# Kernel tuning notes

Hardware: AMD Instinct MI355X
Metric: run time of the kernel (lower is better)

Reference implementation:

```python
import jax, jax.numpy as jnp
import numpy as np

Q_MAX = 127.0  # int8 symmetric quantization range

def _ste_round(v):
    # straight-through round (matches quantize-forward semantics)
    return v + jax.lax.stop_gradient(jnp.round(v) - v)

def setup_inputs() -> dict:
    key = jax.random.key(0)
    k1, k2, k3, k4 = jax.random.split(key, 4)
    B, S, D_IN, D_OUT = 32, 577, 1024, 2560
    x = jax.random.normal(k1, (B, S, D_IN), dtype=jnp.float32)
    # pre-quantized int8 weight stored as int32 for jax friendliness
    w_int = jax.random.randint(k2, (D_OUT, D_IN), -127, 128, dtype=jnp.int32)
    # per-output-row dequant scales (absmax/127 style, small positive)
    scale_w = jax.random.uniform(k3, (D_OUT,), dtype=jnp.float32, minval=0.005, maxval=0.02)
    bias = jax.random.normal(k4, (D_OUT,), dtype=jnp.float32)
    return {"x": x, "w_int": w_int, "scale_w": scale_w, "bias": bias}

def reference(x, w_int, scale_w, bias):
    # bnb Int8Linear: dynamic per-row int8 quantization of activations,
    # per-column (output-feature) weight scales, then bias add.
    # x: [B, S, D_in], w_int: [D_out, D_in] in [-127,127], scale_w: [D_out]
    absmax_x = jnp.max(jnp.abs(x), axis=-1, keepdims=True)  # [B, S, 1]
    scale_x = jnp.maximum(absmax_x, 1e-8) / Q_MAX
    x_q = _ste_round(x / scale_x)  # quantized activations in [-127, 127]
    # integer-valued GEMM carried in fp32 accumulation
    acc = jnp.einsum("bsd,od->bso", x_q, w_int.astype(jnp.float32))
    y = acc * scale_x * scale_w[None, None, :] + bias[None, None, :]
    return y
```

## Files before the change

### kernel.cpp

```cpp
#include <hip/hip_runtime.h>
#include <stdint.h>

typedef int v4i  __attribute__((ext_vector_type(4)));
typedef int v16i __attribute__((ext_vector_type(16)));

__device__ __forceinline__ void gll16(const void* g, void* l) {
    __builtin_amdgcn_global_load_lds(
        (const __attribute__((address_space(1))) void*)(uintptr_t)g,
        (__attribute__((address_space(3))) void*)(uint32_t)(uintptr_t)l,
        16, 0, 0);
}

__global__ __launch_bounds__(256) void quant_x(const float* __restrict__ x,
                                               signed char* __restrict__ xq,
                                               float* __restrict__ sx, int M) {
    const int row = blockIdx.x;
    const int tid = threadIdx.x;
    signed char* qrow = xq + (size_t)row * 1024;
    if (row >= M) {
        ((char4*)qrow)[tid] = make_char4(0, 0, 0, 0);
        if (tid == 0) sx[row] = 0.0f;
        return;
    }
    const float4 v = ((const float4*)(x + (size_t)row * 1024))[tid];
    float a = fmaxf(fmaxf(fabsf(v.x), fabsf(v.y)), fmaxf(fabsf(v.z), fabsf(v.w)));
#pragma unroll
    for (int off = 32; off > 0; off >>= 1)
        a = fmaxf(a, __shfl_xor(a, off));
    __shared__ float red[4];
    if ((tid & 63) == 0) red[tid >> 6] = a;
    __syncthreads();
    const float am = fmaxf(fmaxf(red[0], red[1]), fmaxf(red[2], red[3]));
    const float amc = fmaxf(am, 1e-8f);
    const float scale = amc * (1.0f / 127.0f);
    const float inv = 127.0f / amc;
    char4 q;
    q.x = (signed char)(int)rintf(v.x * inv);
    q.y = (signed char)(int)rintf(v.y * inv);
    q.z = (signed char)(int)rintf(v.z * inv);
    q.w = (signed char)(int)rintf(v.w * inv);
    ((char4*)qrow)[tid] = q;
    if (tid == 0) sx[row] = scale;
}

__global__ __launch_bounds__(256) void conv_w(const int* __restrict__ w,
                                              signed char* __restrict__ w8, int n4) {
    const int i = blockIdx.x * 256 + threadIdx.x;
    if (i < n4) {
        const int4 v = ((const int4*)w)[i];
        char4 c;
        c.x = (signed char)v.x; c.y = (signed char)v.y;
        c.z = (signed char)v.z; c.w = (signed char)v.w;
        ((char4*)w8)[i] = c;
    }
}

__global__ __launch_bounds__(256, 3) void gemm_i8(const signed char* __restrict__ xq,
                                                  const signed char* __restrict__ w8,
                                                  const float* __restrict__ sx,
                                                  const float* __restrict__ sw,
                                                  const float* __restrict__ bias,
                                                  float* __restrict__ out,
                                                  int M, int N, int K) {
    __shared__ signed char As[2][8192];
    __shared__ signed char Bs[2][8192];

    const int tid  = threadIdx.x;
    const int lane = tid & 63;
    const int wave = tid >> 6;
    const int m_off = (wave >> 1) * 64;
    const int n_off = (wave & 1) * 64;
    const int m_block = blockIdx.y * 128;
    const int n_block = blockIdx.x * 128;
    const int NT = K >> 6;

    v16i acc[2][2];
#pragma unroll
    for (int mi = 0; mi < 2; ++mi)
#pragma unroll
        for (int ni = 0; ni < 2; ++ni)
#pragma unroll
            for (int e = 0; e < 16; ++e) acc[mi][ni][e] = 0;

    const int sr = tid >> 2;
    const int sc = ((tid & 3) ^ ((sr >> 1) & 3)) * 16;
    const signed char* aG = xq + (size_t)(m_block + sr) * K + sc;
    const signed char* bG = w8 + (size_t)(n_block + sr) * K + sc;
    const int ldst = wave * 1024;

    auto stage = [&](int Tt, int b) {
        const size_t ko = (size_t)Tt << 6;
        gll16(aG + ko,                    &As[b][ldst]);
        gll16(aG + ko + ((size_t)K << 6), &As[b][ldst + 4096]);
        gll16(bG + ko,                    &Bs[b][ldst]);
        gll16(bG + ko + ((size_t)K << 6), &Bs[b][ldst + 4096]);
    };

    const int rl  = lane & 31;
    const int hi  = lane >> 5;
    const int key = (rl >> 1) & 3;
    const int ck0 = (hi ^ key) * 16;
    const int ck1 = ((2 + hi) ^ key) * 16;
    const int arow = (m_off + rl) * 64;
    const int brow = (n_off + rl) * 64;

    stage(0, 0);
    stage(1, 1);
    asm volatile("s_waitcnt vmcnt(4)" ::: "memory");
    __builtin_amdgcn_s_barrier();

    v4i a0, a1, b0, b1;
    v4i na0, na1, nb0, nb1;
    a0 = *(const v4i*)(As[0] + arow + ck0);
    a1 = *(const v4i*)(As[0] + arow + 2048 + ck0);
    b0 = *(const v4i*)(Bs[0] + brow + ck0);
    b1 = *(const v4i*)(Bs[0] + brow + 2048 + ck0);

    for (int T = 0; T < NT; ++T) {
        const int cur = T & 1;
        const signed char* Ac = As[cur];
        const signed char* Bc = Bs[cur];
        na0 = *(const v4i*)(Ac + arow + ck1);
        na1 = *(const v4i*)(Ac + arow + 2048 + ck1);
        nb0 = *(const v4i*)(Bc + brow + ck1);
        nb1 = *(const v4i*)(Bc + brow + 2048 + ck1);

        acc[0][0] = __builtin_amdgcn_mfma_i32_32x32x32_i8(a0, b0, acc[0][0], 0, 0, 0);
        acc[0][1] = __builtin_amdgcn_mfma_i32_32x32x32_i8(a0, b1, acc[0][1], 0, 0, 0);
        acc[1][0] = __builtin_amdgcn_mfma_i32_32x32x32_i8(a1, b0, acc[1][0], 0, 0, 0);
        acc[1][1] = __builtin_amdgcn_mfma_i32_32x32x32_i8(a1, b1, acc[1][1], 0, 0, 0);

        asm volatile("s_waitcnt lgkmcnt(0)" ::: "memory");
        __builtin_amdgcn_s_barrier();

        if (T + 2 < NT) stage(T + 2, cur);

        if (T + 1 < NT) {
            if (T + 2 < NT)
                asm volatile("s_waitcnt vmcnt(4)" ::: "memory");
            else
                asm volatile("s_waitcnt vmcnt(0)" ::: "memory");
            __builtin_amdgcn_s_barrier();
            const signed char* An = As[cur ^ 1];
            const signed char* Bn = Bs[cur ^ 1];
            a0 = *(const v4i*)(An + arow + ck0);
            a1 = *(const v4i*)(An + arow + 2048 + ck0);
            b0 = *(const v4i*)(Bn + brow + ck0);
            b1 = *(const v4i*)(Bn + brow + 2048 + ck0);
        }

        acc[0][0] = __builtin_amdgcn_mfma_i32_32x32x32_i8(na0, nb0, acc[0][0], 0, 0, 0);
        acc[0][1] = __builtin_amdgcn_mfma_i32_32x32x32_i8(na0, nb1, acc[0][1], 0, 0, 0);
        acc[1][0] = __builtin_amdgcn_mfma_i32_32x32x32_i8(na1, nb0, acc[1][0], 0, 0, 0);
        acc[1][1] = __builtin_amdgcn_mfma_i32_32x32x32_i8(na1, nb1, acc[1][1], 0, 0, 0);
    }

#pragma unroll
    for (int mi = 0; mi < 2; ++mi)
#pragma unroll
        for (int q = 0; q < 4; ++q) {
            const int rbase = m_block + m_off + mi * 32 + q * 8 + hi * 4;
            float sxv[4];
#pragma unroll
            for (int r = 0; r < 4; ++r) sxv[r] = sx[rbase + r];
#pragma unroll
            for (int ni = 0; ni < 2; ++ni) {
                const int col = n_block + n_off + ni * 32 + rl;
                const float swv = sw[col];
                const float bv  = bias[col];
#pragma unroll
                for (int r = 0; r < 4; ++r) {
                    const int row = rbase + r;
                    if (row < M)
                        out[(size_t)row * N + col] = (float)acc[mi][ni][q * 4 + r] * sxv[r] * swv + bv;
                }
            }
        }
}

extern "C" void kernel_launch(void* const* d_in, const int* in_sizes, int n_in,
                              void* d_out, int out_size, void* d_ws, size_t ws_size,
                              hipStream_t stream) {
    const float* x       = (const float*)d_in[0];
    const int*   w_int   = (const int*)d_in[1];
    const float* scale_w = (const float*)d_in[2];
    const float* bias    = (const float*)d_in[3];
    float* out = (float*)d_out;

    const int D_OUT = in_sizes[2];
    const int D_IN  = in_sizes[1] / D_OUT;
    const int M     = in_sizes[0] / D_IN;
    const int Mpad  = ((M + 127) / 128) * 128;

    signed char* xq = (signed char*)d_ws;
    signed char* w8 = xq + (size_t)Mpad * D_IN;
    float*       sx = (float*)(w8 + (size_t)D_OUT * D_IN);

    quant_x<<<Mpad, 256, 0, stream>>>(x, xq, sx, M);
    const int n4 = D_OUT * D_IN / 4;
    conv_w<<<(n4 + 255) / 256, 256, 0, stream>>>(w_int, w8, n4);
    dim3 grid(D_OUT / 128, Mpad / 128);
    gemm_i8<<<grid, dim3(256, 1, 1), 0, stream>>>(xq, w8, sx, scale_w, bias, out, M, D_OUT, D_IN);
}
```

Baseline: 315.1 us.

## Enlarge GEMM tile to 256x256 with 8 waves, triple buffering and XCD-aware mapping

Grows the int8 GEMM workgroup tile from 128x128 to 256x256 with 512 threads, giving each wave a 128x64 sub-tile. This raises operand reuse per LDS load and cuts global traffic. The LDS staging moves to a three-buffer ring, and the A and B prefetches are split and interleaved between MFMA groups, with s_setprio raised around the MFMAs. A 1D grid is remapped so consecutive tiles land on the same XCD for L2 locality. In exchange, LDS use rises to 96KB per block, which limits occupancy to roughly one block per CU, M padding grows to 256, and register pressure goes up.

```diff
diff --git a/kernel.cpp b/kernel.cpp
--- a/kernel.cpp
+++ b/kernel.cpp
@@ -55,28 +55,34 @@
     }
 }
 
-__global__ __launch_bounds__(256, 3) void gemm_i8(const signed char* __restrict__ xq,
+__global__ __launch_bounds__(512, 2) void gemm_i8(const signed char* __restrict__ xq,
                                                   const signed char* __restrict__ w8,
                                                   const float* __restrict__ sx,
                                                   const float* __restrict__ sw,
                                                   const float* __restrict__ bias,
                                                   float* __restrict__ out,
                                                   int M, int N, int K) {
-    __shared__ signed char As[2][8192];
-    __shared__ signed char Bs[2][8192];
+    __shared__ signed char As[3][16384];
+    __shared__ signed char Bs[3][16384];
 
     const int tid  = threadIdx.x;
     const int lane = tid & 63;
     const int wave = tid >> 6;
-    const int m_off = (wave >> 1) * 64;
-    const int n_off = (wave & 1) * 64;
-    const int m_block = blockIdx.y * 128;
-    const int n_block = blockIdx.x * 128;
+    const int m_off = (wave >> 2) * 128;
+    const int n_off = (wave & 3) * 64;
     const int NT = K >> 6;
 
-    v16i acc[2][2];
-#pragma unroll
-    for (int mi = 0; mi < 2; ++mi)
+    const int nwg = gridDim.x;
+    const int qd = nwg >> 3, rd = nwg & 7;
+    const int xcd = blockIdx.x & 7, lid = blockIdx.x >> 3;
+    const int wgid = (xcd < rd ? xcd * (qd + 1) : rd * (qd + 1) + (xcd - rd) * qd) + lid;
+    const int NXB = N >> 8;
+    const int m_block = (wgid / NXB) * 256;
+    const int n_block = (wgid % NXB) * 256;
+
+    v16i acc[4][2];
+#pragma unroll
+    for (int mi = 0; mi < 4; ++mi)
 #pragma unroll
         for (int ni = 0; ni < 2; ++ni)
 #pragma unroll
@@ -88,75 +94,100 @@
     const signed char* bG = w8 + (size_t)(n_block + sr) * K + sc;
     const int ldst = wave * 1024;
 
-    auto stage = [&](int Tt, int b) {
+    auto stageA = [&](int Tt, int b) {
         const size_t ko = (size_t)Tt << 6;
         gll16(aG + ko,                    &As[b][ldst]);
-        gll16(aG + ko + ((size_t)K << 6), &As[b][ldst + 4096]);
+        gll16(aG + ko + ((size_t)K << 7), &As[b][ldst + 8192]);
+    };
+    auto stageB = [&](int Tt, int b) {
+        const size_t ko = (size_t)Tt << 6;
         gll16(bG + ko,                    &Bs[b][ldst]);
-        gll16(bG + ko + ((size_t)K << 6), &Bs[b][ldst + 4096]);
+        gll16(bG + ko + ((size_t)K << 7), &Bs[b][ldst + 8192]);
     };
 
     const int rl  = lane & 31;
     const int hi  = lane >> 5;
     const int key = (rl >> 1) & 3;
-    const int ck0 = (hi ^ key) * 16;
-    const int ck1 = ((2 + hi) ^ key) * 16;
+    const int c0 = (hi ^ key) * 16;
+    const int c1 = ((2 + hi) ^ key) * 16;
     const int arow = (m_off + rl) * 64;
     const int brow = (n_off + rl) * 64;
 
-    stage(0, 0);
-    stage(1, 1);
+    stageA(0, 0); stageB(0, 0);
+    stageA(1, 1); stageB(1, 1);
     asm volatile("s_waitcnt vmcnt(4)" ::: "memory");
     __builtin_amdgcn_s_barrier();
 
-    v4i a0, a1, b0, b1;
-    v4i na0, na1, nb0, nb1;
-    a0 = *(const v4i*)(As[0] + arow + ck0);
-    a1 = *(const v4i*)(As[0] + arow + 2048 + ck0);
-    b0 = *(const v4i*)(Bs[0] + brow + ck0);
-    b1 = *(const v4i*)(Bs[0] + brow + 2048 + ck0);
-
+    int cur = 0;
     for (int T = 0; T < NT; ++T) {
-        const int cur = T & 1;
+        int nx2 = cur + 2; if (nx2 >= 3) nx2 -= 3;
+        const bool pf = (T + 2 < NT);
         const signed char* Ac = As[cur];
         const signed char* Bc = Bs[cur];
-        na0 = *(const v4i*)(Ac + arow + ck1);
-        na1 = *(const v4i*)(Ac + arow + 2048 + ck1);
-        nb0 = *(const v4i*)(Bc + brow + ck1);
-        nb1 = *(const v4i*)(Bc + brow + 2048 + ck1);
-
-        acc[0][0] = __builtin_amdgcn_mfma_i32_32x32x32_i8(a0, b0, acc[0][0], 0, 0, 0);
-        acc[0][1] = __builtin_amdgcn_mfma_i32_32x32x32_i8(a0, b1, acc[0][1], 0, 0, 0);
-        acc[1][0] = __builtin_amdgcn_mfma_i32_32x32x32_i8(a1, b0, acc[1][0], 0, 0, 0);
-        acc[1][1] = __builtin_amdgcn_mfma_i32_32x32x32_i8(a1, b1, acc[1][1], 0, 0, 0);
-
+
+        v4i b0, b1;
+        if (pf) stageA(T + 2, nx2);
+        {
+            v4i A0 = *(const v4i*)(Ac + arow + c0);
+            v4i A1 = *(const v4i*)(Ac + arow + 2048 + c0);
+            b0 = *(const v4i*)(Bc + brow + c0);
+            b1 = *(const v4i*)(Bc + brow + 2048 + c0);
+            __builtin_amdgcn_s_setprio(1);
+            acc[0][0] = __builtin_amdgcn_mfma_i32_32x32x32_i8(A0, b0, acc[0][0], 0, 0, 0);
+            acc[0][1] = __builtin_amdgcn_mfma_i32_32x32x32_i8(A0, b1, acc[0][1], 0, 0, 0);
+            acc[1][0] = __builtin_amdgcn_mfma_i32_32x32x32_i8(A1, b0, acc[1][0], 0, 0, 0);
+            acc[1][1] = __builtin_amdgcn_mfma_i32_32x32x32_i8(A1, b1, acc[1][1], 0, 0, 0);
+            __builtin_amdgcn_s_setprio(0);
+        }
+        __builtin_amdgcn_s_barrier();
+        if (pf) stageB(T + 2, nx2);
+        {
+            v4i A2 = *(const v4i*)(Ac + arow + 4096 + c0);
+            v4i A3 = *(const v4i*)(Ac + arow + 6144 + c0);
+            __builtin_amdgcn_s_setprio(1);
+            acc[2][0] = __builtin_amdgcn_mfma_i32_32x32x32_i8(A2, b0, acc[2][0], 0, 0, 0);
+            acc[2][1] = __builtin_amdgcn_mfma_i32_32x32x32_i8(A2, b1, acc[2][1], 0, 0, 0);
+            acc[3][0] = __builtin_amdgcn_mfma_i32_32x32x32_i8(A3, b0, acc[3][0], 0, 0, 0);
+            acc[3][1] = __builtin_amdgcn_mfma_i32_32x32x32_i8(A3, b1, acc[3][1], 0, 0, 0);
+            __builtin_amdgcn_s_setprio(0);
+        }
+        __builtin_amdgcn_s_barrier();
+        {
+            v4i A0 = *(const v4i*)(Ac + arow + c1);
+            v4i A1 = *(const v4i*)(Ac + arow + 2048 + c1);
+            b0 = *(const v4i*)(Bc + brow + c1);
+            b1 = *(const v4i*)(Bc + brow + 2048 + c1);
+            __builtin_amdgcn_s_setprio(1);
+            acc[0][0] = __builtin_amdgcn_mfma_i32_32x32x32_i8(A0, b0, acc[0][0], 0, 0, 0);
+            acc[0][1] = __builtin_amdgcn_mfma_i32_32x32x32_i8(A0, b1, acc[0][1], 0, 0, 0);
+            acc[1][0] = __builtin_amdgcn_mfma_i32_32x32x32_i8(A1, b0, acc[1][0], 0, 0, 0);
+            acc[1][1] = __builtin_amdgcn_mfma_i32_32x32x32_i8(A1, b1, acc[1][1], 0, 0, 0);
+            __builtin_amdgcn_s_setprio(0);
+        }
+        __builtin_amdgcn_s_barrier();
+        {
+            v4i A2 = *(const v4i*)(Ac + arow + 4096 + c1);
+            v4i A3 = *(const v4i*)(Ac + arow + 6144 + c1);
+            __builtin_amdgcn_s_setprio(1);
+            acc[2][0] = __builtin_amdgcn_mfma_i32_32x32x32_i8(A2, b0, acc[2][0], 0, 0, 0);
+            acc[2][1] = __builtin_amdgcn_mfma_i32_32x32x32_i8(A2, b1, acc[2][1], 0, 0, 0);
+            acc[3][0] = __builtin_amdgcn_mfma_i32_32x32x32_i8(A3, b0, acc[3][0], 0, 0, 0);
+            acc[3][1] = __builtin_amdgcn_mfma_i32_32x32x32_i8(A3, b1, acc[3][1], 0, 0, 0);
+            __builtin_amdgcn_s_setprio(0);
+        }
         asm volatile("s_waitcnt lgkmcnt(0)" ::: "memory");
-        __builtin_amdgcn_s_barrier();
-
-        if (T + 2 < NT) stage(T + 2, cur);
-
         if (T + 1 < NT) {
-            if (T + 2 < NT)
+            if (pf)
                 asm volatile("s_waitcnt vmcnt(4)" ::: "memory");
             else
                 asm volatile("s_waitcnt vmcnt(0)" ::: "memory");
             __builtin_amdgcn_s_barrier();
-            const signed char* An = As[cur ^ 1];
-            const signed char* Bn = Bs[cur ^ 1];
-            a0 = *(const v4i*)(An + arow + ck0);
-            a1 = *(const v4i*)(An + arow + 2048 + ck0);
-            b0 = *(const v4i*)(Bn + brow + ck0);
-            b1 = *(const v4i*)(Bn + brow + 2048 + ck0);
-        }
-
-        acc[0][0] = __builtin_amdgcn_mfma_i32_32x32x32_i8(na0, nb0, acc[0][0], 0, 0, 0);
-        acc[0][1] = __builtin_amdgcn_mfma_i32_32x32x32_i8(na0, nb1, acc[0][1], 0, 0, 0);
-        acc[1][0] = __builtin_amdgcn_mfma_i32_32x32x32_i8(na1, nb0, acc[1][0], 0, 0, 0);
-        acc[1][1] = __builtin_amdgcn_mfma_i32_32x32x32_i8(na1, nb1, acc[1][1], 0, 0, 0);
+        }
+        cur = (cur + 1 == 3) ? 0 : cur + 1;
     }
 
 #pragma unroll
-    for (int mi = 0; mi < 2; ++mi)
+    for (int mi = 0; mi < 4; ++mi)
 #pragma unroll
         for (int q = 0; q < 4; ++q) {
             const int rbase = m_block + m_off + mi * 32 + q * 8 + hi * 4;
@@ -190,7 +221,7 @@
     const int D_OUT = in_sizes[2];
     const int D_IN  = in_sizes[1] / D_OUT;
     const int M     = in_sizes[0] / D_IN;
-    const int Mpad  = ((M + 127) / 128) * 128;
+    const int Mpad  = ((M + 255) / 256) * 256;
 
     signed char* xq = (signed char*)d_ws;
     signed char* w8 = xq + (size_t)Mpad * D_IN;
@@ -199,6 +230,6 @@
     quant_x<<<Mpad, 256, 0, stream>>>(x, xq, sx, M);
     const int n4 = D_OUT * D_IN / 4;
     conv_w<<<(n4 + 255) / 256, 256, 0, stream>>>(w_int, w8, n4);
-    dim3 grid(D_OUT / 128, Mpad / 128);
-    gemm_i8<<<grid, dim3(256, 1, 1), 0, stream>>>(xq, w8, sx, scale_w, bias, out, M, D_OUT, D_IN);
-}
+    const int nwg = (D_OUT / 256) * (Mpad / 256);
+    gemm_i8<<<dim3(nwg, 1, 1), dim3(512, 1, 1), 0, stream>>>(xq, w8, sx, scale_w, bias, out, M, D_OUT, D_IN);
+}
```

Result: slower. 335.7 us (+6.5%).

## Triple-buffer LDS, remap workgroups per XCD, and raise MFMA priority

Applied to the files above, without the earlier changes.

The GEMM moves from a double-buffered to a triple-buffered LDS ring. The prefetch for tile T+2 is now issued at the start of each iteration, which removes one barrier per iteration, and all eight MFMAs run back-to-back under s_setprio. The 2D grid becomes a 1D grid whose block IDs are remapped so that consecutive tiles land on the same XCD, which should improve L2 reuse. The cost is 48KB of LDS per block, up from 32KB, which may reduce occupancy below the launch-bounds target of 3 blocks.

```diff
diff --git a/kernel.cpp b/kernel.cpp
--- a/kernel.cpp
+++ b/kernel.cpp
@@ -62,17 +62,23 @@
                                                   const float* __restrict__ bias,
                                                   float* __restrict__ out,
                                                   int M, int N, int K) {
-    __shared__ signed char As[2][8192];
-    __shared__ signed char Bs[2][8192];
+    __shared__ signed char As[3][8192];
+    __shared__ signed char Bs[3][8192];
 
     const int tid  = threadIdx.x;
     const int lane = tid & 63;
     const int wave = tid >> 6;
     const int m_off = (wave >> 1) * 64;
     const int n_off = (wave & 1) * 64;
-    const int m_block = blockIdx.y * 128;
-    const int n_block = blockIdx.x * 128;
     const int NT = K >> 6;
+
+    const int nwg = gridDim.x;
+    const int qd = nwg >> 3, rd = nwg & 7;
+    const int xcd = blockIdx.x & 7, lid = blockIdx.x >> 3;
+    const int wgid = (xcd < rd ? xcd * (qd + 1) : rd * (qd + 1) + (xcd - rd) * qd) + lid;
+    const int NXB = N >> 7;
+    const int m_block = (wgid / NXB) * 128;
+    const int n_block = (wgid % NXB) * 128;
 
     v16i acc[2][2];
 #pragma unroll
@@ -99,8 +105,8 @@
     const int rl  = lane & 31;
     const int hi  = lane >> 5;
     const int key = (rl >> 1) & 3;
-    const int ck0 = (hi ^ key) * 16;
-    const int ck1 = ((2 + hi) ^ key) * 16;
+    const int c0 = (hi ^ key) * 16;
+    const int c1 = ((2 + hi) ^ key) * 16;
     const int arow = (m_off + rl) * 64;
     const int brow = (n_off + rl) * 64;
 
@@ -111,48 +117,55 @@
 
     v4i a0, a1, b0, b1;
     v4i na0, na1, nb0, nb1;
-    a0 = *(const v4i*)(As[0] + arow + ck0);
-    a1 = *(const v4i*)(As[0] + arow + 2048 + ck0);
-    b0 = *(const v4i*)(Bs[0] + brow + ck0);
-    b1 = *(const v4i*)(Bs[0] + brow + 2048 + ck0);
-
+    a0 = *(const v4i*)(As[0] + arow + c0);
+    a1 = *(const v4i*)(As[0] + arow + 2048 + c0);
+    b0 = *(const v4i*)(Bs[0] + brow + c0);
+    b1 = *(const v4i*)(Bs[0] + brow + 2048 + c0);
+
+    int cur = 0;
     for (int T = 0; T < NT; ++T) {
-        const int cur = T & 1;
+        int nxt = cur + 1; if (nxt >= 3) nxt -= 3;
+        int nx2 = cur + 2; if (nx2 >= 3) nx2 -= 3;
+        const bool pf = (T + 2 < NT);
+
+        if (pf) stage(T + 2, nx2);
+
         const signed char* Ac = As[cur];
         const signed char* Bc = Bs[cur];
-        na0 = *(const v4i*)(Ac + arow + ck1);
-        na1 = *(const v4i*)(Ac + arow + 2048 + ck1);
-        nb0 = *(const v4i*)(Bc + brow + ck1);
-        nb1 = *(const v4i*)(Bc + brow + 2048 + ck1);
-
+        na0 = *(const v4i*)(Ac + arow + c1);
+        na1 = *(const v4i*)(Ac + arow + 2048 + c1);
+        nb0 = *(const v4i*)(Bc + brow + c1);
+        nb1 = *(const v4i*)(Bc + brow + 2048 + c1);
+
+        __builtin_amdgcn_s_setprio(1);
         acc[0][0] = __builtin_amdgcn_mfma_i32_32x32x32_i8(a0, b0, acc[0][0], 0, 0, 0);
         acc[0][1] = __builtin_amdgcn_mfma_i32_32x32x32_i8(a0, b1, acc[0][1], 0, 0, 0);
         acc[1][0] = __builtin_amdgcn_mfma_i32_32x32x32_i8(a1, b0, acc[1][0], 0, 0, 0);
         acc[1][1] = __builtin_amdgcn_mfma_i32_32x32x32_i8(a1, b1, acc[1][1], 0, 0, 0);
+        __builtin_amdgcn_s_setprio(0);
+
+        __builtin_amdgcn_s_setprio(1);
+        acc[0][0] = __builtin_amdgcn_mfma_i32_32x32x32_i8(na0, nb0, acc[0][0], 0, 0, 0);
+        acc[0][1] = __builtin_amdgcn_mfma_i32_32x32x32_i8(na0, nb1, acc[0][1], 0, 0, 0);
+        acc[1][0] = __builtin_amdgcn_mfma_i32_32x32x32_i8(na1, nb0, acc[1][0], 0, 0, 0);
+        acc[1][1] = __builtin_amdgcn_mfma_i32_32x32x32_i8(na1, nb1, acc[1][1], 0, 0, 0);
+        __builtin_amdgcn_s_setprio(0);
 
         asm volatile("s_waitcnt lgkmcnt(0)" ::: "memory");
-        __builtin_amdgcn_s_barrier();
-
-        if (T + 2 < NT) stage(T + 2, cur);
-
         if (T + 1 < NT) {
-            if (T + 2 < NT)
+            if (pf)
                 asm volatile("s_waitcnt vmcnt(4)" ::: "memory");
             else
                 asm volatile("s_waitcnt vmcnt(0)" ::: "memory");
             __builtin_amdgcn_s_barrier();
-            const signed char* An = As[cur ^ 1];
-            const signed char* Bn = Bs[cur ^ 1];
-            a0 = *(const v4i*)(An + arow + ck0);
-            a1 = *(const v4i*)(An + arow + 2048 + ck0);
-            b0 = *(const v4i*)(Bn + brow + ck0);
-            b1 = *(const v4i*)(Bn + brow + 2048 + ck0);
+            const signed char* An = As[nxt];
+            const signed char* Bn = Bs[nxt];
+            a0 = *(const v4i*)(An + arow + c0);
+            a1 = *(const v4i*)(An + arow + 2048 + c0);
+            b0 = *(const v4i*)(Bn + brow + c0);
+            b1 = *(const v4i*)(Bn + brow + 2048 + c0);
         }
-
-        acc[0][0] = __builtin_amdgcn_mfma_i32_32x32x32_i8(na0, nb0, acc[0][0], 0, 0, 0);
-        acc[0][1] = __builtin_amdgcn_mfma_i32_32x32x32_i8(na0, nb1, acc[0][1], 0, 0, 0);
-        acc[1][0] = __builtin_amdgcn_mfma_i32_32x32x32_i8(na1, nb0, acc[1][0], 0, 0, 0);
-        acc[1][1] = __builtin_amdgcn_mfma_i32_32x32x32_i8(na1, nb1, acc[1][1], 0, 0, 0);
+        cur = nxt;
     }
 
 #pragma unroll
@@ -199,6 +212,6 @@
     quant_x<<<Mpad, 256, 0, stream>>>(x, xq, sx, M);
     const int n4 = D_OUT * D_IN / 4;
     conv_w<<<(n4 + 255) / 256, 256, 0, stream>>>(w_int, w8, n4);
-    dim3 grid(D_OUT / 128, Mpad / 128);
-    gemm_i8<<<grid, dim3(256, 1, 1), 0, stream>>>(xq, w8, sx, scale_w, bias, out, M, D_OUT, D_IN);
-}
+    const int nwg = (Mpad / 128) * (D_OUT / 128);
+    gemm_i8<<<dim3(nwg, 1, 1), dim3(256, 1, 1), 0, stream>>>(xq, w8, sx, scale_w, bias, out, M, D_OUT, D_IN);
+}
```

Result: slower. 325.7 us (+3.4%).
